# Optimization experiments

Hardware: AMD Instinct MI355X
Metric: run time of the kernel (lower is better)

Reference implementation:

```python
import jax, jax.numpy as jnp
import numpy as np

NUM_EXPERTS = 64
IN_FEATURES = 1024
TOP_K = 2
MAX_REL_TOKENS = 8 * TOP_K / NUM_EXPERTS  # expert_capacity * k / num_experts = 0.25
HIGH_NEGATIVE = -100000.0
B = 131072


def topk_mask(x, k, axis, replacement):
    # torch.quantile with q = 1 - k/n, linear interpolation (jnp default)
    n = x.shape[axis]
    q = 1.0 - k / n
    quant = jnp.quantile(x, q, axis=axis, keepdims=True)
    return jnp.where(x > quant, x, replacement)


def setup_inputs() -> dict:
    key = jax.random.key(0)
    k1, k2, k3, k4 = jax.random.split(key, 4)
    x = jax.random.normal(k1, (B, IN_FEATURES), dtype=jnp.float32)
    noise = jax.random.normal(k2, (B, NUM_EXPERTS), dtype=jnp.float32)
    W = jax.random.normal(k3, (NUM_EXPERTS, IN_FEATURES), dtype=jnp.float32) * (1.0 / np.sqrt(IN_FEATURES))
    b = jax.random.normal(k4, (NUM_EXPERTS,), dtype=jnp.float32) * 0.01
    return {"x": x, "noise": noise, "W": W, "b": b}


def reference(x, noise, W, b):
    # flatten(start_dim=1) is identity for 2D input; linear gate + gaussian noise (std=0.1)
    logits = jnp.einsum("bf,ef->be", x, W) + b + 0.1 * noise  # [B, E]
    # capacity mask: per-expert (column) top-max_tokens over the batch dim
    max_tokens = max(int(logits.shape[0] * MAX_REL_TOKENS), 1)
    logits = topk_mask(logits, max_tokens, axis=0, replacement=HIGH_NEGATIVE)
    # expert mask: per-token top-k over experts
    logits = topk_mask(logits, TOP_K, axis=1, replacement=HIGH_NEGATIVE)
    return jax.nn.softmax(logits, axis=1)
```

## Files before the change

kernel.cpp:

```cpp
#include <hip/hip_runtime.h>
#include <math.h>

#define NTOK 131072
#define NEXP 64
#define KDIM 1024
#define NBINS 4096
#define CAP 8192
#define RLO 98303u
#define RHI 98304u

__device__ __forceinline__ int bin_of(float v) {
    int bn = (int)floorf((v + 8.0f) * 256.0f);
    bn = bn < 0 ? 0 : bn;
    bn = bn > (NBINS - 1) ? (NBINS - 1) : bn;
    return bn;
}

__global__ void transpose_w_kernel(const float* __restrict__ W, float* __restrict__ Wt) {
    int idx = blockIdx.x * 256 + threadIdx.x;
    int k = idx >> 6, e = idx & 63;
    Wt[k * 64 + e] = W[e * 1024 + k];
}

__global__ __launch_bounds__(256, 2)
void gemm_kernel(const float* __restrict__ x, const float* __restrict__ noise,
                 const float* __restrict__ Wt, const float* __restrict__ b,
                 float* __restrict__ logits, unsigned int* __restrict__ hist) {
    __shared__ float4 xs4[64 * 33];
    __shared__ float4 wt4[128 * 16];

    const int tid = threadIdx.x;
    const int tx = tid & 15;
    const int ty = tid >> 4;
    const long t0 = (long)blockIdx.x * 64;

    float4 acc[4];
    acc[0] = acc[1] = acc[2] = acc[3] = make_float4(0.f, 0.f, 0.f, 0.f);

    const int st_t  = tid >> 5;
    const int st_kk = tid & 31;
    const int wk    = tid >> 4;
    const int we4   = tid & 15;

    for (int kt = 0; kt < KDIM; kt += 128) {
        __syncthreads();
        #pragma unroll
        for (int c = 0; c < 8; ++c) {
            int tt = st_t + c * 8;
            xs4[tt * 33 + st_kk] =
                reinterpret_cast<const float4*>(x + (t0 + tt) * 1024 + kt)[st_kk];
        }
        #pragma unroll
        for (int c = 0; c < 8; ++c) {
            int kk = wk + c * 16;
            wt4[kk * 16 + we4] =
                reinterpret_cast<const float4*>(Wt + (long)(kt + kk) * 64)[we4];
        }
        __syncthreads();
        const float* xs = reinterpret_cast<const float*>(xs4);
        const int xbase = 4 * ty * 132;
        #pragma unroll 8
        for (int k = 0; k < 128; ++k) {
            float4 wv = wt4[k * 16 + tx];
            float x0 = xs[xbase + k];
            float x1 = xs[xbase + 132 + k];
            float x2 = xs[xbase + 264 + k];
            float x3 = xs[xbase + 396 + k];
            acc[0].x += x0 * wv.x; acc[0].y += x0 * wv.y; acc[0].z += x0 * wv.z; acc[0].w += x0 * wv.w;
            acc[1].x += x1 * wv.x; acc[1].y += x1 * wv.y; acc[1].z += x1 * wv.z; acc[1].w += x1 * wv.w;
            acc[2].x += x2 * wv.x; acc[2].y += x2 * wv.y; acc[2].z += x2 * wv.z; acc[2].w += x2 * wv.w;
            acc[3].x += x3 * wv.x; acc[3].y += x3 * wv.y; acc[3].z += x3 * wv.z; acc[3].w += x3 * wv.w;
        }
    }
    const float4 bb = reinterpret_cast<const float4*>(b)[tx];
    #pragma unroll
    for (int i = 0; i < 4; ++i) {
        long t = t0 + 4 * ty + i;
        float4 nz = reinterpret_cast<const float4*>(noise + t * 64)[tx];
        float4 r;
        r.x = acc[i].x + bb.x + 0.1f * nz.x;
        r.y = acc[i].y + bb.y + 0.1f * nz.y;
        r.z = acc[i].z + bb.z + 0.1f * nz.z;
        r.w = acc[i].w + bb.w + 0.1f * nz.w;
        reinterpret_cast<float4*>(logits + t * 64)[tx] = r;
        int e0 = 4 * tx;
        atomicAdd(&hist[(e0 + 0) * NBINS + bin_of(r.x)], 1u);
        atomicAdd(&hist[(e0 + 1) * NBINS + bin_of(r.y)], 1u);
        atomicAdd(&hist[(e0 + 2) * NBINS + bin_of(r.z)], 1u);
        atomicAdd(&hist[(e0 + 3) * NBINS + bin_of(r.w)], 1u);
    }
}

__global__ void find_bins_kernel(const unsigned int* __restrict__ hist,
                                 int* __restrict__ blo, int* __restrict__ bhi,
                                 int* __restrict__ basearr) {
    __shared__ unsigned int psum[256];
    const int e = blockIdx.x, tid = threadIdx.x;
    const unsigned int* h = hist + e * NBINS;
    unsigned int loc[16];
    unsigned int s = 0;
    #pragma unroll
    for (int i = 0; i < 16; ++i) { loc[i] = h[tid * 16 + i]; s += loc[i]; }
    psum[tid] = s;
    __syncthreads();
    for (int off = 1; off < 256; off <<= 1) {
        unsigned int vv = (tid >= off) ? psum[tid - off] : 0u;
        __syncthreads();
        psum[tid] += vv;
        __syncthreads();
    }
    unsigned int cum = (tid == 0) ? 0u : psum[tid - 1];
    #pragma unroll
    for (int i = 0; i < 16; ++i) {
        unsigned int nb = cum + loc[i];
        if (cum <= RLO && RLO < nb) { blo[e] = tid * 16 + i; basearr[e] = (int)cum; }
        if (cum <= RHI && RHI < nb) { bhi[e] = tid * 16 + i; }
        cum = nb;
    }
}

__global__ void extract_kernel(const float* __restrict__ logits,
                               const int* __restrict__ blo, const int* __restrict__ bhi,
                               unsigned int* __restrict__ cnt, float* __restrict__ cand) {
    int i = blockIdx.x * 256 + threadIdx.x;
    float v = logits[i];
    int e = i & 63;
    int bn = bin_of(v);
    if (bn >= blo[e] && bn <= bhi[e]) {
        unsigned int p = atomicAdd(&cnt[e], 1u);
        if (p < CAP) cand[e * CAP + p] = v;
    }
}

__global__ void cuts_kernel(const float* __restrict__ cand, const unsigned int* __restrict__ cnt,
                            const int* __restrict__ basearr, float* __restrict__ cut) {
    __shared__ float s[CAP];
    const int e = blockIdx.x, tid = threadIdx.x;
    int n = (int)min(cnt[e], (unsigned int)CAP);
    int np2 = 2; while (np2 < n) np2 <<= 1;
    for (int i = tid; i < np2; i += 256) s[i] = (i < n) ? cand[e * CAP + i] : 3.0e38f;
    __syncthreads();
    for (int k = 2; k <= np2; k <<= 1) {
        for (int j = k >> 1; j > 0; j >>= 1) {
            for (int i = tid; i < np2; i += 256) {
                int ixj = i ^ j;
                if (ixj > i) {
                    float a = s[i], bb = s[ixj];
                    bool up = ((i & k) == 0);
                    if (up ? (a > bb) : (a < bb)) { s[i] = bb; s[ixj] = a; }
                }
            }
            __syncthreads();
        }
    }
    if (tid == 0) {
        int base = basearr[e];
        int r1 = (int)RLO - base, r2 = (int)RHI - base;
        r1 = max(0, min(r1, np2 - 1));
        r2 = max(0, min(r2, np2 - 1));
        float s1 = s[r1], s2 = s[r2];
        cut[e] = s1 + 0.25f * (s2 - s1);
    }
}

__device__ __forceinline__ float wave_max_f(float v) {
    #pragma unroll
    for (int off = 32; off > 0; off >>= 1) v = fmaxf(v, __shfl_xor(v, off));
    return v;
}
__device__ __forceinline__ float wave_sum_f(float v) {
    #pragma unroll
    for (int off = 32; off > 0; off >>= 1) v += __shfl_xor(v, off);
    return v;
}
__device__ __forceinline__ double wave_max_d(double v) {
    #pragma unroll
    for (int off = 32; off > 0; off >>= 1) { double o = __shfl_xor(v, off); v = (o > v) ? o : v; }
    return v;
}
__device__ __forceinline__ double wave_sum_d(double v) {
    #pragma unroll
    for (int off = 32; off > 0; off >>= 1) v += __shfl_xor(v, off);
    return v;
}

__global__ __launch_bounds__(256)
void finalize_kernel(const float* __restrict__ logits, const float* __restrict__ cut,
                     const float* __restrict__ x, const float* __restrict__ W,
                     const float* __restrict__ noise, const float* __restrict__ b,
                     float* __restrict__ out) {
    const int tid = threadIdx.x;
    const int lane = tid & 63;
    const long row = (long)blockIdx.x * 4 + (tid >> 6);
    const float c = cut[lane];
    const float v = logits[row * 64 + lane];
    float m = (v > c) ? v : -100000.0f;

    float v1 = wave_max_f(m);
    unsigned long long b1m = __ballot(m == v1);
    int l1 = __ffsll((unsigned long long)b1m) - 1;
    float mm = (lane == l1) ? -INFINITY : m;
    float v2 = wave_max_f(mm);
    unsigned long long b2m = __ballot(mm == v2);
    int l2 = __ffsll((unsigned long long)b2m) - 1;
    float mmm = (lane == l2) ? -INFINITY : mm;
    float v3 = wave_max_f(mmm);

    float qr = v3 + 0.03125f * (v2 - v3);
    bool kept = m > qr;
    int cntk = __popcll(__ballot(kept));
    bool risky = (cntk != 2) || (v2 - v3 < 1e-4f);

    if (!risky) {
        float ex = kept ? expf(m - v1) : 0.0f;
        float Z = wave_sum_f(ex);
        out[row * 64 + lane] = ex / Z;
        return;
    }
    const float* xr = x + row * 1024;
    const float* wr = W + (long)lane * 1024;
    double a0 = 0.0, a1 = 0.0, a2 = 0.0, a3 = 0.0;
    for (int k = 0; k < 1024; k += 4) {
        a0 += (double)xr[k + 0] * (double)wr[k + 0];
        a1 += (double)xr[k + 1] * (double)wr[k + 1];
        a2 += (double)xr[k + 2] * (double)wr[k + 2];
        a3 += (double)xr[k + 3] * (double)wr[k + 3];
    }
    double lg = ((a0 + a1) + (a2 + a3)) + (double)b[lane] + 0.1 * (double)noise[row * 64 + lane];
    double md = (lg > (double)c) ? lg : -100000.0;
    double d1 = wave_max_d(md);
    unsigned long long db1 = __ballot(md == d1);
    int dl1 = __ffsll((unsigned long long)db1) - 1;
    double md2 = (lane == dl1) ? -(double)INFINITY : md;
    double d2 = wave_max_d(md2);
    unsigned long long db2 = __ballot(md2 == d2);
    int dl2 = __ffsll((unsigned long long)db2) - 1;
    double md3 = (lane == dl2) ? -(double)INFINITY : md2;
    double d3 = wave_max_d(md3);
    double qrd = d3 + 0.03125 * (d2 - d3);
    bool kd = md > qrd;
    int cd = __popcll(__ballot(kd));
    double od;
    if (cd == 0) od = 1.0 / 64.0;
    else {
        double exd = kd ? exp(md - d1) : 0.0;
        double Zd = wave_sum_d(exd);
        od = exd / Zd;
    }
    out[row * 64 + lane] = (float)od;
}

extern "C" void kernel_launch(void* const* d_in, const int* in_sizes, int n_in,
                              void* d_out, int out_size, void* d_ws, size_t ws_size,
                              hipStream_t stream) {
    const float* x     = (const float*)d_in[0];
    const float* noise = (const float*)d_in[1];
    const float* W     = (const float*)d_in[2];
    const float* b     = (const float*)d_in[3];
    float* out = (float*)d_out;

    char* ws = (char*)d_ws;
    float*        Wt      = (float*)(ws + 0);
    unsigned int* hist    = (unsigned int*)(ws + 262144);
    unsigned int* cnt     = (unsigned int*)(ws + 1310720);
    int*          blo     = (int*)(ws + 1310976);
    int*          bhi     = (int*)(ws + 1311232);
    int*          basearr = (int*)(ws + 1311488);
    float*        cut     = (float*)(ws + 1311744);
    float*        cand    = (float*)(ws + 1312000);

    hipMemsetAsync(hist, 0, 1048576 + 256, stream);

    hipLaunchKernelGGL(transpose_w_kernel, dim3(256), dim3(256), 0, stream, W, Wt);
    hipLaunchKernelGGL(gemm_kernel, dim3(NTOK / 64), dim3(256), 0, stream,
                       x, noise, Wt, b, out, hist);
    hipLaunchKernelGGL(find_bins_kernel, dim3(64), dim3(256), 0, stream,
                       hist, blo, bhi, basearr);
    hipLaunchKernelGGL(extract_kernel, dim3((NTOK * NEXP) / 256), dim3(256), 0, stream,
                       out, blo, bhi, cnt, cand);
    hipLaunchKernelGGL(cuts_kernel, dim3(64), dim3(256), 0, stream,
                       cand, cnt, basearr, cut);
    hipLaunchKernelGGL(finalize_kernel, dim3(NTOK / 4), dim3(256), 0, stream,
                       out, cut, x, W, noise, b, out);
}
```

Baseline: 1.362 ms.

## Double-buffer GEMM tiles with direct global-to-LDS loads and larger register tiles

Rewrites the gate GEMM to use 256-token blocks of 128 threads, each computing a 16x8 register tile, with K staged in 16-wide chunks through double-buffered LDS filled by global_load_lds with an XOR swizzle. The goal is to overlap global loads with FMA work and raise arithmetic intensity per LDS read. The W transpose now goes through shared memory for coalescing. The cost is a large accumulator register footprint at one block per CU-slot launch bound, and fewer threads per block, which may reduce occupancy and latency hiding.

```diff
diff --git a/kernel.cpp b/kernel.cpp
--- a/kernel.cpp
+++ b/kernel.cpp
@@ -9,6 +9,9 @@
 #define RLO 98303u
 #define RHI 98304u
 
+#define TT 256
+#define BK 16
+
 __device__ __forceinline__ int bin_of(float v) {
     int bn = (int)floorf((v + 8.0f) * 256.0f);
     bn = bn < 0 ? 0 : bn;
@@ -16,78 +19,139 @@
     return bn;
 }
 
+__device__ __forceinline__ void gl_lds16(const void* g, void* l) {
+    __builtin_amdgcn_global_load_lds((const __attribute__((address_space(1))) void*)g,
+                                     (__attribute__((address_space(3))) void*)l,
+                                     16, 0, 0);
+}
+
 __global__ void transpose_w_kernel(const float* __restrict__ W, float* __restrict__ Wt) {
-    int idx = blockIdx.x * 256 + threadIdx.x;
-    int k = idx >> 6, e = idx & 63;
-    Wt[k * 64 + e] = W[e * 1024 + k];
-}
-
-__global__ __launch_bounds__(256, 2)
+    __shared__ float tile[64][65];
+    const int bk = blockIdx.x * 64;
+    const int j = threadIdx.x & 63, i = threadIdx.x >> 6;
+    #pragma unroll
+    for (int r = 0; r < 16; ++r) {
+        int e = 4 * r + i;
+        tile[e][j] = W[e * 1024 + bk + j];
+    }
+    __syncthreads();
+    #pragma unroll
+    for (int r = 0; r < 16; ++r) {
+        int k = 4 * r + i;
+        Wt[(long)(bk + k) * 64 + j] = tile[j][k];
+    }
+}
+
+__device__ __forceinline__ void stage_tile(const float* __restrict__ x,
+                                           const float* __restrict__ Wt,
+                                           long tb, int kt, int tid,
+                                           float4* xbuf, float4* wbuf) {
+    #pragma unroll
+    for (int s = 0; s < 8; ++s) {
+        int q = s * 128 + tid;
+        int t = s * 32 + (tid >> 2);
+        int c = (tid & 3) ^ ((2 * s + (tid >> 6)) & 3);
+        const float* g = x + (tb + t) * 1024 + kt + 4 * c;
+        gl_lds16(g, (void*)(xbuf + q));
+    }
+    #pragma unroll
+    for (int s = 0; s < 2; ++s) {
+        int q = s * 128 + tid;
+        const float* g = Wt + (long)kt * 64 + q * 4;
+        gl_lds16(g, (void*)(wbuf + q));
+    }
+}
+
+__device__ __forceinline__ void compute_tile(const float4* __restrict__ xb,
+                                             const float4* __restrict__ wb,
+                                             float acc[16][8], int tx, int ty) {
+    #pragma unroll
+    for (int c = 0; c < 4; ++c) {
+        const int cp = c ^ (ty & 3);
+        float4 xv[16];
+        #pragma unroll
+        for (int j = 0; j < 16; ++j) xv[j] = xb[64 * ty + 4 * j + cp];
+        #pragma unroll
+        for (int kk = 0; kk < 4; ++kk) {
+            float4 w0 = wb[(4 * c + kk) * 16 + 2 * tx];
+            float4 w1 = wb[(4 * c + kk) * 16 + 2 * tx + 1];
+            #pragma unroll
+            for (int j = 0; j < 16; ++j) {
+                float xx = (kk == 0) ? xv[j].x : (kk == 1) ? xv[j].y
+                         : (kk == 2) ? xv[j].z : xv[j].w;
+                acc[j][0] = fmaf(xx, w0.x, acc[j][0]);
+                acc[j][1] = fmaf(xx, w0.y, acc[j][1]);
+                acc[j][2] = fmaf(xx, w0.z, acc[j][2]);
+                acc[j][3] = fmaf(xx, w0.w, acc[j][3]);
+                acc[j][4] = fmaf(xx, w1.x, acc[j][4]);
+                acc[j][5] = fmaf(xx, w1.y, acc[j][5]);
+                acc[j][6] = fmaf(xx, w1.z, acc[j][6]);
+                acc[j][7] = fmaf(xx, w1.w, acc[j][7]);
+            }
+        }
+    }
+}
+
+__global__ __launch_bounds__(128, 1)
 void gemm_kernel(const float* __restrict__ x, const float* __restrict__ noise,
                  const float* __restrict__ Wt, const float* __restrict__ b,
                  float* __restrict__ logits, unsigned int* __restrict__ hist) {
-    __shared__ float4 xs4[64 * 33];
-    __shared__ float4 wt4[128 * 16];
+    __shared__ float4 ldsX[2][1024];
+    __shared__ float4 ldsW[2][256];
 
     const int tid = threadIdx.x;
-    const int tx = tid & 15;
-    const int ty = tid >> 4;
-    const long t0 = (long)blockIdx.x * 64;
-
-    float4 acc[4];
-    acc[0] = acc[1] = acc[2] = acc[3] = make_float4(0.f, 0.f, 0.f, 0.f);
-
-    const int st_t  = tid >> 5;
-    const int st_kk = tid & 31;
-    const int wk    = tid >> 4;
-    const int we4   = tid & 15;
-
-    for (int kt = 0; kt < KDIM; kt += 128) {
+    const int tx = tid & 7;
+    const int ty = tid >> 3;
+    const long tb = (long)blockIdx.x * TT;
+
+    float acc[16][8];
+    #pragma unroll
+    for (int j = 0; j < 16; ++j)
+        #pragma unroll
+        for (int e = 0; e < 8; ++e) acc[j][e] = 0.0f;
+
+    stage_tile(x, Wt, tb, 0, tid, ldsX[0], ldsW[0]);
+
+    #pragma unroll 1
+    for (int it = 0; it < KDIM / (2 * BK); ++it) {
+        int kt = it * 2 * BK;
         __syncthreads();
-        #pragma unroll
-        for (int c = 0; c < 8; ++c) {
-            int tt = st_t + c * 8;
-            xs4[tt * 33 + st_kk] =
-                reinterpret_cast<const float4*>(x + (t0 + tt) * 1024 + kt)[st_kk];
-        }
-        #pragma unroll
-        for (int c = 0; c < 8; ++c) {
-            int kk = wk + c * 16;
-            wt4[kk * 16 + we4] =
-                reinterpret_cast<const float4*>(Wt + (long)(kt + kk) * 64)[we4];
-        }
+        if (kt + BK < KDIM) stage_tile(x, Wt, tb, kt + BK, tid, ldsX[1], ldsW[1]);
+        compute_tile(ldsX[0], ldsW[0], acc, tx, ty);
         __syncthreads();
-        const float* xs = reinterpret_cast<const float*>(xs4);
-        const int xbase = 4 * ty * 132;
-        #pragma unroll 8
-        for (int k = 0; k < 128; ++k) {
-            float4 wv = wt4[k * 16 + tx];
-            float x0 = xs[xbase + k];
-            float x1 = xs[xbase + 132 + k];
-            float x2 = xs[xbase + 264 + k];
-            float x3 = xs[xbase + 396 + k];
-            acc[0].x += x0 * wv.x; acc[0].y += x0 * wv.y; acc[0].z += x0 * wv.z; acc[0].w += x0 * wv.w;
-            acc[1].x += x1 * wv.x; acc[1].y += x1 * wv.y; acc[1].z += x1 * wv.z; acc[1].w += x1 * wv.w;
-            acc[2].x += x2 * wv.x; acc[2].y += x2 * wv.y; acc[2].z += x2 * wv.z; acc[2].w += x2 * wv.w;
-            acc[3].x += x3 * wv.x; acc[3].y += x3 * wv.y; acc[3].z += x3 * wv.z; acc[3].w += x3 * wv.w;
-        }
-    }
-    const float4 bb = reinterpret_cast<const float4*>(b)[tx];
-    #pragma unroll
-    for (int i = 0; i < 4; ++i) {
-        long t = t0 + 4 * ty + i;
-        float4 nz = reinterpret_cast<const float4*>(noise + t * 64)[tx];
-        float4 r;
-        r.x = acc[i].x + bb.x + 0.1f * nz.x;
-        r.y = acc[i].y + bb.y + 0.1f * nz.y;
-        r.z = acc[i].z + bb.z + 0.1f * nz.z;
-        r.w = acc[i].w + bb.w + 0.1f * nz.w;
-        reinterpret_cast<float4*>(logits + t * 64)[tx] = r;
-        int e0 = 4 * tx;
-        atomicAdd(&hist[(e0 + 0) * NBINS + bin_of(r.x)], 1u);
-        atomicAdd(&hist[(e0 + 1) * NBINS + bin_of(r.y)], 1u);
-        atomicAdd(&hist[(e0 + 2) * NBINS + bin_of(r.z)], 1u);
-        atomicAdd(&hist[(e0 + 3) * NBINS + bin_of(r.w)], 1u);
+        if (kt + 2 * BK < KDIM) stage_tile(x, Wt, tb, kt + 2 * BK, tid, ldsX[0], ldsW[0]);
+        compute_tile(ldsX[1], ldsW[1], acc, tx, ty);
+    }
+
+    const float4* b4 = (const float4*)b;
+    const float4 bb0 = b4[2 * tx], bb1 = b4[2 * tx + 1];
+    const float4* noise4 = (const float4*)noise;
+    float4* logits4 = (float4*)logits;
+    const int e0 = 8 * tx;
+    #pragma unroll 1
+    for (int j = 0; j < 16; ++j) {
+        long t = tb + 16 * ty + j;
+        float4 nz0 = noise4[t * 16 + 2 * tx];
+        float4 nz1 = noise4[t * 16 + 2 * tx + 1];
+        float4 r0, r1;
+        r0.x = acc[j][0] + bb0.x + 0.1f * nz0.x;
+        r0.y = acc[j][1] + bb0.y + 0.1f * nz0.y;
+        r0.z = acc[j][2] + bb0.z + 0.1f * nz0.z;
+        r0.w = acc[j][3] + bb0.w + 0.1f * nz0.w;
+        r1.x = acc[j][4] + bb1.x + 0.1f * nz1.x;
+        r1.y = acc[j][5] + bb1.y + 0.1f * nz1.y;
+        r1.z = acc[j][6] + bb1.z + 0.1f * nz1.z;
+        r1.w = acc[j][7] + bb1.w + 0.1f * nz1.w;
+        logits4[t * 16 + 2 * tx] = r0;
+        logits4[t * 16 + 2 * tx + 1] = r1;
+        atomicAdd(&hist[(e0 + 0) * NBINS + bin_of(r0.x)], 1u);
+        atomicAdd(&hist[(e0 + 1) * NBINS + bin_of(r0.y)], 1u);
+        atomicAdd(&hist[(e0 + 2) * NBINS + bin_of(r0.z)], 1u);
+        atomicAdd(&hist[(e0 + 3) * NBINS + bin_of(r0.w)], 1u);
+        atomicAdd(&hist[(e0 + 4) * NBINS + bin_of(r1.x)], 1u);
+        atomicAdd(&hist[(e0 + 5) * NBINS + bin_of(r1.y)], 1u);
+        atomicAdd(&hist[(e0 + 6) * NBINS + bin_of(r1.z)], 1u);
+        atomicAdd(&hist[(e0 + 7) * NBINS + bin_of(r1.w)], 1u);
     }
 }
 
@@ -271,8 +335,8 @@
 
     hipMemsetAsync(hist, 0, 1048576 + 256, stream);
 
-    hipLaunchKernelGGL(transpose_w_kernel, dim3(256), dim3(256), 0, stream, W, Wt);
-    hipLaunchKernelGGL(gemm_kernel, dim3(NTOK / 64), dim3(256), 0, stream,
+    hipLaunchKernelGGL(transpose_w_kernel, dim3(16), dim3(256), 0, stream, W, Wt);
+    hipLaunchKernelGGL(gemm_kernel, dim3(NTOK / TT), dim3(128), 0, stream,
                        x, noise, Wt, b, out, hist);
     hipLaunchKernelGGL(find_bins_kernel, dim3(64), dim3(256), 0, stream,
                        hist, blo, bhi, basearr);
```

Result: slower. 4.563 ms (+234.9%).
